# Optimization experiments

Measured on AMD Instinct MI355X. Metric: run time of the kernel, lower is better.

Reference implementation:

```python
import jax, jax.numpy as jnp
import numpy as np

EPS_LOG = 1e-07
EPS_LN = 1e-05


def layer_norm(x, gamma, beta):
    mu = jnp.mean(x, axis=-1, keepdims=True)
    var = jnp.mean((x - mu) ** 2, axis=-1, keepdims=True)
    return (x - mu) * jax.lax.rsqrt(var + EPS_LN) * gamma + beta


def setup_inputs() -> dict:
    key = jax.random.key(0)
    ks = jax.random.split(key, 20)
    N, D_IN, H = 500000, 39, 256
    inp = {"x": jax.random.uniform(ks[0], (N, D_IN), dtype=jnp.float32)}
    # fc1: 39 -> 256
    inp["W1"] = jax.random.normal(ks[1], (H, D_IN), dtype=jnp.float32) * (1.0 / np.sqrt(D_IN))
    inp["b1"] = jnp.zeros((H,), dtype=jnp.float32)
    # fc2..fc7: 256 -> 256
    for i in range(2, 8):
        inp[f"W{i}"] = jax.random.normal(ks[i], (H, H), dtype=jnp.float32) * (1.0 / np.sqrt(H))
        inp[f"b{i}"] = jnp.zeros((H,), dtype=jnp.float32)
    # fc8: 256 -> 1
    inp["W8"] = jax.random.normal(ks[8], (1, H), dtype=jnp.float32) * (1.0 / np.sqrt(H))
    inp["b8"] = jnp.zeros((1,), dtype=jnp.float32)
    # shared LayerNorm affine params
    inp["gamma"] = jnp.ones((H,), dtype=jnp.float32)
    inp["beta"] = jnp.zeros((H,), dtype=jnp.float32)
    return inp


def reference(x, W1, b1, W2, b2, W3, b3, W4, b4, W5, b5, W6, b6, W7, b7, W8, b8, gamma, beta):
    h = 0.1 * jnp.log(x + EPS_LOG)
    h = jnp.tanh(h @ W1.T + b1)
    for W, b in ((W2, b2), (W3, b3), (W4, b4), (W5, b5), (W6, b6), (W7, b7)):
        h = jax.nn.elu(layer_norm(h, gamma, beta) @ W.T + b)
    return layer_norm(h, gamma, beta) @ W8.T + b8
```

## Files before the change

kernel.cpp:

```cpp
#include <hip/hip_runtime.h>

typedef _Float16 f16;
typedef _Float16 f16x8 __attribute__((ext_vector_type(8)));
typedef float f32x4 __attribute__((ext_vector_type(4)));

#define N_ROWS 500000
#define EPS_LOG 1e-7f
#define EPS_LN  1e-5f

#define CST_BYTE_OFF 20480

__global__ void prep_kernel(const float* __restrict__ W1,
                            const float* __restrict__ W2, const float* __restrict__ W3,
                            const float* __restrict__ W4, const float* __restrict__ W5,
                            const float* __restrict__ W6, const float* __restrict__ W7,
                            const float* __restrict__ b2, const float* __restrict__ b3,
                            const float* __restrict__ b4, const float* __restrict__ b5,
                            const float* __restrict__ b6, const float* __restrict__ b7,
                            const float* __restrict__ gamma, const float* __restrict__ beta,
                            f16* __restrict__ ws) {
  float* cstF = (float*)((char*)ws + CST_BYTE_OFF);
  int idx = blockIdx.x * 256 + threadIdx.x;
  if (idx < 10240) {
    int j = idx / 40, k = idx - j * 40;
    ws[idx] = (f16)((k < 39) ? W1[j * 39 + k] : 0.0f);
  } else if (idx < 16384) {
  } else if (idx < 409600) {
    int o = idx - 16384;
    int li = o >> 16;  o &= 65535;
    const float* W = (li == 0) ? W2 : (li == 1) ? W3 : (li == 2) ? W4
                   : (li == 3) ? W5 : (li == 4) ? W6 : W7;
    int e = o & 7, j = (o >> 3) & 255, kgrp = (o >> 11) & 3, kt = o >> 13;
    int k = kt * 32 + kgrp * 8 + e;
    ws[idx] = (f16)(W[j * 256 + k] * gamma[k]);
  } else if (idx < 411136) {
    int o = idx - 409600;
    int li = o >> 8, j = o & 255;
    const float* W = (li == 0) ? W2 : (li == 1) ? W3 : (li == 2) ? W4
                   : (li == 3) ? W5 : (li == 4) ? W6 : W7;
    const float* b = (li == 0) ? b2 : (li == 1) ? b3 : (li == 2) ? b4
                   : (li == 3) ? b5 : (li == 4) ? b6 : b7;
    float sg = 0.f, bb = 0.f;
    for (int k = 0; k < 256; ++k) {
      float w = W[j * 256 + k];
      sg += w * gamma[k];
      bb += w * beta[k];
    }
    cstF[li * 256 + j] = sg;
    cstF[1536 + li * 256 + j] = bb + b[j];
  }
}

__global__ __launch_bounds__(256, 2)
void mlp_kernel(const float* __restrict__ x, const f16* __restrict__ wsw,
                const float* __restrict__ b1, const float* __restrict__ W8,
                const float* __restrict__ b8, const float* __restrict__ gamma,
                const float* __restrict__ beta, float* __restrict__ out) {
  __shared__ __attribute__((aligned(16))) f16 hbuf[128 * 256];
  __shared__ __attribute__((aligned(16))) f16 wslab[8192];

  const float* cstF = (const float*)((const char*)wsw + CST_BYTE_OFF);
  const int t = threadIdx.x;
  const int lane = t & 63;
  const int wid = t >> 6;
  const int lm = lane & 15;
  const int lg = lane >> 4;
  const long rowbase = (long)blockIdx.x * 128;
  const int R0 = wid * 32;
  const int myrow0 = R0 + lm;
  const int myrow1 = R0 + 16 + lm;
  const int sA0 = ((myrow0 >> 1) & 7) << 3;
  const int sA1 = ((myrow1 >> 1) & 7) << 3;

  f16x8 ld0, ld1, ld2, ld3;
  auto slab_load = [&](const f16* g) {
    ld0 = *(const f16x8*)(g + (0 * 256 + t) * 8);
    ld1 = *(const f16x8*)(g + (1 * 256 + t) * 8);
    ld2 = *(const f16x8*)(g + (2 * 256 + t) * 8);
    ld3 = *(const f16x8*)(g + (3 * 256 + t) * 8);
  };
  auto slab_write = [&]() {
    *(f16x8*)&wslab[(0 * 256 + t) * 8] = ld0;
    *(f16x8*)&wslab[(1 * 256 + t) * 8] = ld1;
    *(f16x8*)&wslab[(2 * 256 + t) * 8] = ld2;
    *(f16x8*)&wslab[(3 * 256 + t) * 8] = ld3;
  };

  const f16* WgBase = wsw + 16384;
  slab_load(WgBase);

  #pragma unroll 1
  for (int i = 0; i < 32; ++i) {
    int r = R0 + i;
    long gr = rowbase + r;
    float tv = 0.0f;
    if (lane < 39) {
      float xv = (gr < N_ROWS) ? x[gr * 39 + lane] : 1.0f;
      tv = 0.1f * __logf(xv + EPS_LOG);
    }
    hbuf[r * 256 + (lane ^ (((r >> 1) & 7) << 3))] = (f16)tv;
  }

  f32x4 acc0[16], acc1[16];

  auto do_tile = [&](f32x4* acc, int rbase, bool tanh_act, const float* cvec) {
    float nm[4] = {0, 0, 0, 0}, nq[4] = {0, 0, 0, 0};
    #pragma unroll
    for (int nt = 0; nt < 16; ++nt) {
      float c0 = cvec[nt * 16 + lm];
      #pragma unroll
      for (int i = 0; i < 4; ++i) {
        float v = acc[nt][i] + c0;
        float a;
        if (tanh_act) {
          float e2 = __expf(2.f * v);
          a = 1.f - 2.f / (e2 + 1.f);
        } else {
          a = (v > 0.f) ? v : (__expf(v) - 1.f);
        }
        acc[nt][i] = a;
        nm[i] += a;
        nq[i] = fmaf(a, a, nq[i]);
      }
    }
    #pragma unroll
    for (int off = 1; off < 16; off <<= 1) {
      #pragma unroll
      for (int i = 0; i < 4; ++i) {
        nm[i] += __shfl_xor(nm[i], off, 64);
        nq[i] += __shfl_xor(nq[i], off, 64);
      }
    }
    float mu[4], is_[4];
    #pragma unroll
    for (int i = 0; i < 4; ++i) {
      float m = nm[i] * (1.f / 256.f);
      float var = nq[i] * (1.f / 256.f) - m * m;
      mu[i] = m;
      is_[i] = rsqrtf(var + EPS_LN);
    }
    #pragma unroll
    for (int nt = 0; nt < 16; ++nt) {
      int col = nt * 16 + lm;
      #pragma unroll
      for (int i = 0; i < 4; ++i) {
        int r = rbase + lg * 4 + i;
        hbuf[r * 256 + (col ^ (((r >> 1) & 7) << 3))] =
            (f16)((acc[nt][i] - mu[i]) * is_[i]);
      }
    }
  };

  {
    #pragma unroll
    for (int i = 0; i < 16; ++i) { acc0[i] = (f32x4){0,0,0,0}; acc1[i] = (f32x4){0,0,0,0}; }
    #pragma unroll
    for (int kt = 0; kt < 2; ++kt) {
      f16x8 av0 = *(const f16x8*)&hbuf[myrow0 * 256 + ((kt * 32 + lg * 8) ^ sA0)];
      f16x8 av1 = *(const f16x8*)&hbuf[myrow1 * 256 + ((kt * 32 + lg * 8) ^ sA1)];
      #pragma unroll
      for (int nt = 0; nt < 16; ++nt) {
        int j40 = (nt * 16 + lm) * 40;
        f16x8 bf = 0;
        if (kt == 0)       bf = *(const f16x8*)&wsw[j40 + lg * 8];
        else if (lg == 0)  bf = *(const f16x8*)&wsw[j40 + 32];
        acc0[nt] = __builtin_amdgcn_mfma_f32_16x16x32_f16(av0, bf, acc0[nt], 0, 0, 0);
        acc1[nt] = __builtin_amdgcn_mfma_f32_16x16x32_f16(av1, bf, acc1[nt], 0, 0, 0);
      }
    }
    do_tile(acc0, R0,      true, b1);
    do_tile(acc1, R0 + 16, true, b1);
  }

  #pragma unroll 1
  for (int li = 0; li < 6; ++li) {
    #pragma unroll
    for (int i = 0; i < 16; ++i) { acc0[i] = (f32x4){0,0,0,0}; acc1[i] = (f32x4){0,0,0,0}; }
    #pragma unroll 1
    for (int kt = 0; kt < 8; ++kt) {
      slab_write();
      if (kt < 7)       slab_load(WgBase + li * 65536 + (kt + 1) * 8192);
      else if (li < 5)  slab_load(WgBase + (li + 1) * 65536);
      __syncthreads();
      {
        f16x8 av0 = *(const f16x8*)&hbuf[myrow0 * 256 + ((kt * 32 + lg * 8) ^ sA0)];
        f16x8 av1 = *(const f16x8*)&hbuf[myrow1 * 256 + ((kt * 32 + lg * 8) ^ sA1)];
        #pragma unroll
        for (int nt = 0; nt < 16; ++nt) {
          f16x8 bf = *(const f16x8*)&wslab[lg * 2048 + (nt * 16 + lm) * 8];
          acc0[nt] = __builtin_amdgcn_mfma_f32_16x16x32_f16(av0, bf, acc0[nt], 0, 0, 0);
          acc1[nt] = __builtin_amdgcn_mfma_f32_16x16x32_f16(av1, bf, acc1[nt], 0, 0, 0);
        }
      }
      __syncthreads();
    }
    do_tile(acc0, R0,      false, cstF + 1536 + li * 256);
    do_tile(acc1, R0 + 16, false, cstF + 1536 + li * 256);
  }

  {
    float wg8[16], be8 = 0.f;
    #pragma unroll
    for (int j = 0; j < 16; ++j) {
      int c = lm * 16 + j;
      float w = W8[c];
      wg8[j] = w * gamma[c];
      be8 = fmaf(w, beta[c], be8);
    }
    #pragma unroll
    for (int off = 1; off < 16; off <<= 1) be8 += __shfl_xor(be8, off, 64);
    float cb8 = be8 + b8[0];
    #pragma unroll
    for (int tile = 0; tile < 2; ++tile) {
      #pragma unroll
      for (int i = 0; i < 4; ++i) {
        int r = R0 + tile * 16 + lg * 4 + i;
        int s3 = ((r >> 1) & 7) << 3;
        f16x8 h0 = *(const f16x8*)&hbuf[r * 256 + ((lm * 16) ^ s3)];
        f16x8 h1 = *(const f16x8*)&hbuf[r * 256 + ((lm * 16 + 8) ^ s3)];
        float d = 0.f;
        #pragma unroll
        for (int j = 0; j < 8; ++j) d = fmaf((float)h0[j], wg8[j], d);
        #pragma unroll
        for (int j = 0; j < 8; ++j) d = fmaf((float)h1[j], wg8[8 + j], d);
        #pragma unroll
        for (int off = 1; off < 16; off <<= 1) d += __shfl_xor(d, off, 64);
        if (lm == 0) {
          long gr = rowbase + r;
          if (gr < N_ROWS) out[gr] = d + cb8;
        }
      }
    }
  }
}

extern "C" void kernel_launch(void* const* d_in, const int* in_sizes, int n_in,
                              void* d_out, int out_size, void* d_ws, size_t ws_size,
                              hipStream_t stream) {
  const float* x  = (const float*)d_in[0];
  const float* W1 = (const float*)d_in[1];
  const float* b1 = (const float*)d_in[2];
  const float* W2 = (const float*)d_in[3];
  const float* b2 = (const float*)d_in[4];
  const float* W3 = (const float*)d_in[5];
  const float* b3 = (const float*)d_in[6];
  const float* W4 = (const float*)d_in[7];
  const float* b4 = (const float*)d_in[8];
  const float* W5 = (const float*)d_in[9];
  const float* b5 = (const float*)d_in[10];
  const float* W6 = (const float*)d_in[11];
  const float* b6 = (const float*)d_in[12];
  const float* W7 = (const float*)d_in[13];
  const float* b7 = (const float*)d_in[14];
  const float* W8 = (const float*)d_in[15];
  const float* b8 = (const float*)d_in[16];
  const float* gm = (const float*)d_in[17];
  const float* bt = (const float*)d_in[18];
  f16* ws = (f16*)d_ws;
  float* out = (float*)d_out;

  prep_kernel<<<1606, 256, 0, stream>>>(W1, W2, W3, W4, W5, W6, W7,
                                        b2, b3, b4, b5, b6, b7, gm, bt, ws);

  int nblk = (N_ROWS + 127) / 128;
  mlp_kernel<<<nblk, 256, 0, stream>>>(x, ws, b1, W8, b8, gm, bt, out);
}
```

Before: 1.034 ms.

## Transpose MFMA operands so LayerNorm stats reduce per-lane and fuse final projection

```diff
diff --git a/kernel.cpp b/kernel.cpp
--- a/kernel.cpp
+++ b/kernel.cpp
@@ -1,6 +1,7 @@
 #include <hip/hip_runtime.h>
 
 typedef _Float16 f16;
+typedef _Float16 f16x4 __attribute__((ext_vector_type(4)));
 typedef _Float16 f16x8 __attribute__((ext_vector_type(8)));
 typedef float f32x4 __attribute__((ext_vector_type(4)));
 
@@ -14,6 +15,7 @@
                             const float* __restrict__ W2, const float* __restrict__ W3,
                             const float* __restrict__ W4, const float* __restrict__ W5,
                             const float* __restrict__ W6, const float* __restrict__ W7,
+                            const float* __restrict__ W8, const float* __restrict__ b8,
                             const float* __restrict__ b2, const float* __restrict__ b3,
                             const float* __restrict__ b4, const float* __restrict__ b5,
                             const float* __restrict__ b6, const float* __restrict__ b7,
@@ -40,22 +42,27 @@
                    : (li == 3) ? W5 : (li == 4) ? W6 : W7;
     const float* b = (li == 0) ? b2 : (li == 1) ? b3 : (li == 2) ? b4
                    : (li == 3) ? b5 : (li == 4) ? b6 : b7;
-    float sg = 0.f, bb = 0.f;
+    float bb = 0.f;
+    for (int k = 0; k < 256; ++k) bb = fmaf(W[j * 256 + k], beta[k], bb);
+    cstF[1536 + li * 256 + j] = bb + b[j];
+  } else if (idx < 411392) {
+    int j = idx - 411136;
+    cstF[j] = W8[j] * gamma[j];
+  } else if (idx == 411392) {
+    float s8 = 0.f, cb = 0.f;
     for (int k = 0; k < 256; ++k) {
-      float w = W[j * 256 + k];
-      sg += w * gamma[k];
-      bb += w * beta[k];
-    }
-    cstF[li * 256 + j] = sg;
-    cstF[1536 + li * 256 + j] = bb + b[j];
+      float w = W8[k];
+      s8 = fmaf(w, gamma[k], s8);
+      cb = fmaf(w, beta[k], cb);
+    }
+    cstF[256] = s8;
+    cstF[257] = cb + b8[0];
   }
 }
 
-__global__ __launch_bounds__(256, 2)
+__global__ __launch_bounds__(256, 1)
 void mlp_kernel(const float* __restrict__ x, const f16* __restrict__ wsw,
-                const float* __restrict__ b1, const float* __restrict__ W8,
-                const float* __restrict__ b8, const float* __restrict__ gamma,
-                const float* __restrict__ beta, float* __restrict__ out) {
+                const float* __restrict__ b1, float* __restrict__ out) {
   __shared__ __attribute__((aligned(16))) f16 hbuf[128 * 256];
   __shared__ __attribute__((aligned(16))) f16 wslab[8192];
 
@@ -67,10 +74,10 @@
   const int lg = lane >> 4;
   const long rowbase = (long)blockIdx.x * 128;
   const int R0 = wid * 32;
-  const int myrow0 = R0 + lm;
-  const int myrow1 = R0 + 16 + lm;
-  const int sA0 = ((myrow0 >> 1) & 7) << 3;
-  const int sA1 = ((myrow1 >> 1) & 7) << 3;
+  const int row0 = R0 + lm;
+  const int row1 = R0 + 16 + lm;
+  const int sw0 = (row0 & 7) << 3;
+  const int sw1 = (row1 & 7) << 3;
 
   f16x8 ld0, ld1, ld2, ld3;
   auto slab_load = [&](const f16* g) {
@@ -98,19 +105,19 @@
       float xv = (gr < N_ROWS) ? x[gr * 39 + lane] : 1.0f;
       tv = 0.1f * __logf(xv + EPS_LOG);
     }
-    hbuf[r * 256 + (lane ^ (((r >> 1) & 7) << 3))] = (f16)tv;
+    hbuf[r * 256 + (lane ^ ((r & 7) << 3))] = (f16)tv;
   }
 
   f32x4 acc0[16], acc1[16];
 
-  auto do_tile = [&](f32x4* acc, int rbase, bool tanh_act, const float* cvec) {
-    float nm[4] = {0, 0, 0, 0}, nq[4] = {0, 0, 0, 0};
-    #pragma unroll
-    for (int nt = 0; nt < 16; ++nt) {
-      float c0 = cvec[nt * 16 + lm];
+  auto do_tile = [&](f32x4* acc, int rt, bool tanh_act, const float* cvec) {
+    float nm = 0.f, nq = 0.f;
+    #pragma unroll
+    for (int jt = 0; jt < 16; ++jt) {
+      f32x4 c4 = *(const f32x4*)&cvec[jt * 16 + lg * 4];
       #pragma unroll
       for (int i = 0; i < 4; ++i) {
-        float v = acc[nt][i] + c0;
+        float v = acc[jt][i] + c4[i];
         float a;
         if (tanh_act) {
           float e2 = __expf(2.f * v);
@@ -118,36 +125,52 @@
         } else {
           a = (v > 0.f) ? v : (__expf(v) - 1.f);
         }
-        acc[nt][i] = a;
-        nm[i] += a;
-        nq[i] = fmaf(a, a, nq[i]);
-      }
-    }
-    #pragma unroll
-    for (int off = 1; off < 16; off <<= 1) {
+        acc[jt][i] = a;
+        nm += a;
+        nq = fmaf(a, a, nq);
+      }
+    }
+    nm += __shfl_xor(nm, 16, 64);  nq += __shfl_xor(nq, 16, 64);
+    nm += __shfl_xor(nm, 32, 64);  nq += __shfl_xor(nq, 32, 64);
+    float mu = nm * (1.f / 256.f);
+    float is = rsqrtf(nq * (1.f / 256.f) - mu * mu + EPS_LN);
+    int row = R0 + rt * 16 + lm;
+    int sw = (row & 7) << 3;
+    #pragma unroll
+    for (int jt = 0; jt < 16; ++jt) {
+      f16x4 z4;
+      #pragma unroll
+      for (int i = 0; i < 4; ++i) z4[i] = (f16)((acc[jt][i] - mu) * is);
+      *(f16x4*)&hbuf[row * 256 + ((jt * 16 + lg * 4) ^ sw)] = z4;
+    }
+  };
+
+  auto final_tile = [&](f32x4* acc, int rt) {
+    const float* bb7 = cstF + 1536 + 5 * 256;
+    float s8 = cstF[256], cb8 = cstF[257];
+    float nm = 0.f, nq = 0.f, dt = 0.f;
+    #pragma unroll
+    for (int jt = 0; jt < 16; ++jt) {
+      f32x4 c4 = *(const f32x4*)&bb7[jt * 16 + lg * 4];
+      f32x4 w4 = *(const f32x4*)&cstF[jt * 16 + lg * 4];
       #pragma unroll
       for (int i = 0; i < 4; ++i) {
-        nm[i] += __shfl_xor(nm[i], off, 64);
-        nq[i] += __shfl_xor(nq[i], off, 64);
-      }
-    }
-    float mu[4], is_[4];
-    #pragma unroll
-    for (int i = 0; i < 4; ++i) {
-      float m = nm[i] * (1.f / 256.f);
-      float var = nq[i] * (1.f / 256.f) - m * m;
-      mu[i] = m;
-      is_[i] = rsqrtf(var + EPS_LN);
-    }
-    #pragma unroll
-    for (int nt = 0; nt < 16; ++nt) {
-      int col = nt * 16 + lm;
-      #pragma unroll
-      for (int i = 0; i < 4; ++i) {
-        int r = rbase + lg * 4 + i;
-        hbuf[r * 256 + (col ^ (((r >> 1) & 7) << 3))] =
-            (f16)((acc[nt][i] - mu[i]) * is_[i]);
-      }
+        float v = acc[jt][i] + c4[i];
+        float a = (v > 0.f) ? v : (__expf(v) - 1.f);
+        nm += a;
+        nq = fmaf(a, a, nq);
+        dt = fmaf(a, w4[i], dt);
+      }
+    }
+    nm += __shfl_xor(nm, 16, 64);  nq += __shfl_xor(nq, 16, 64);
+    dt += __shfl_xor(dt, 16, 64);
+    nm += __shfl_xor(nm, 32, 64);  nq += __shfl_xor(nq, 32, 64);
+    dt += __shfl_xor(dt, 32, 64);
+    float mu = nm * (1.f / 256.f);
+    float is = rsqrtf(nq * (1.f / 256.f) - mu * mu + EPS_LN);
+    if (lane < 16) {
+      long gr = rowbase + R0 + rt * 16 + lm;
+      if (gr < N_ROWS) out[gr] = fmaf(is, dt - mu * s8, cb8);
     }
   };
 
@@ -156,20 +179,20 @@
     for (int i = 0; i < 16; ++i) { acc0[i] = (f32x4){0,0,0,0}; acc1[i] = (f32x4){0,0,0,0}; }
     #pragma unroll
     for (int kt = 0; kt < 2; ++kt) {
-      f16x8 av0 = *(const f16x8*)&hbuf[myrow0 * 256 + ((kt * 32 + lg * 8) ^ sA0)];
-      f16x8 av1 = *(const f16x8*)&hbuf[myrow1 * 256 + ((kt * 32 + lg * 8) ^ sA1)];
-      #pragma unroll
-      for (int nt = 0; nt < 16; ++nt) {
-        int j40 = (nt * 16 + lm) * 40;
-        f16x8 bf = 0;
-        if (kt == 0)       bf = *(const f16x8*)&wsw[j40 + lg * 8];
-        else if (lg == 0)  bf = *(const f16x8*)&wsw[j40 + 32];
-        acc0[nt] = __builtin_amdgcn_mfma_f32_16x16x32_f16(av0, bf, acc0[nt], 0, 0, 0);
-        acc1[nt] = __builtin_amdgcn_mfma_f32_16x16x32_f16(av1, bf, acc1[nt], 0, 0, 0);
-      }
-    }
-    do_tile(acc0, R0,      true, b1);
-    do_tile(acc1, R0 + 16, true, b1);
+      f16x8 bv0 = *(const f16x8*)&hbuf[row0 * 256 + ((kt * 32 + lg * 8) ^ sw0)];
+      f16x8 bv1 = *(const f16x8*)&hbuf[row1 * 256 + ((kt * 32 + lg * 8) ^ sw1)];
+      #pragma unroll
+      for (int jt = 0; jt < 16; ++jt) {
+        int j40 = (jt * 16 + lm) * 40;
+        f16x8 af = 0;
+        if (kt == 0)       af = *(const f16x8*)&wsw[j40 + lg * 8];
+        else if (lg == 0)  af = *(const f16x8*)&wsw[j40 + 32];
+        acc0[jt] = __builtin_amdgcn_mfma_f32_16x16x32_f16(af, bv0, acc0[jt], 0, 0, 0);
+        acc1[jt] = __builtin_amdgcn_mfma_f32_16x16x32_f16(af, bv1, acc1[jt], 0, 0, 0);
+      }
+    }
+    do_tile(acc0, 0, true, b1);
+    do_tile(acc1, 1, true, b1);
   }
 
   #pragma unroll 1
@@ -183,53 +206,23 @@
       else if (li < 5)  slab_load(WgBase + (li + 1) * 65536);
       __syncthreads();
       {
-        f16x8 av0 = *(const f16x8*)&hbuf[myrow0 * 256 + ((kt * 32 + lg * 8) ^ sA0)];
-        f16x8 av1 = *(const f16x8*)&hbuf[myrow1 * 256 + ((kt * 32 + lg * 8) ^ sA1)];
+        f16x8 bv0 = *(const f16x8*)&hbuf[row0 * 256 + ((kt * 32 + lg * 8) ^ sw0)];
+        f16x8 bv1 = *(const f16x8*)&hbuf[row1 * 256 + ((kt * 32 + lg * 8) ^ sw1)];
         #pragma unroll
-        for (int nt = 0; nt < 16; ++nt) {
-          f16x8 bf = *(const f16x8*)&wslab[lg * 2048 + (nt * 16 + lm) * 8];
-          acc0[nt] = __builtin_amdgcn_mfma_f32_16x16x32_f16(av0, bf, acc0[nt], 0, 0, 0);
-          acc1[nt] = __builtin_amdgcn_mfma_f32_16x16x32_f16(av1, bf, acc1[nt], 0, 0, 0);
+        for (int jt = 0; jt < 16; ++jt) {
+          f16x8 af = *(const f16x8*)&wslab[lg * 2048 + (jt * 16 + lm) * 8];
+          acc0[jt] = __builtin_amdgcn_mfma_f32_16x16x32_f16(af, bv0, acc0[jt], 0, 0, 0);
+          acc1[jt] = __builtin_amdgcn_mfma_f32_16x16x32_f16(af, bv1, acc1[jt], 0, 0, 0);
         }
       }
       __syncthreads();
     }
-    do_tile(acc0, R0,      false, cstF + 1536 + li * 256);
-    do_tile(acc1, R0 + 16, false, cstF + 1536 + li * 256);
-  }
-
-  {
-    float wg8[16], be8 = 0.f;
-    #pragma unroll
-    for (int j = 0; j < 16; ++j) {
-      int c = lm * 16 + j;
-      float w = W8[c];
-      wg8[j] = w * gamma[c];
-      be8 = fmaf(w, beta[c], be8);
-    }
-    #pragma unroll
-    for (int off = 1; off < 16; off <<= 1) be8 += __shfl_xor(be8, off, 64);
-    float cb8 = be8 + b8[0];
-    #pragma unroll
-    for (int tile = 0; tile < 2; ++tile) {
-      #pragma unroll
-      for (int i = 0; i < 4; ++i) {
-        int r = R0 + tile * 16 + lg * 4 + i;
-        int s3 = ((r >> 1) & 7) << 3;
-        f16x8 h0 = *(const f16x8*)&hbuf[r * 256 + ((lm * 16) ^ s3)];
-        f16x8 h1 = *(const f16x8*)&hbuf[r * 256 + ((lm * 16 + 8) ^ s3)];
-        float d = 0.f;
-        #pragma unroll
-        for (int j = 0; j < 8; ++j) d = fmaf((float)h0[j], wg8[j], d);
-        #pragma unroll
-        for (int j = 0; j < 8; ++j) d = fmaf((float)h1[j], wg8[8 + j], d);
-        #pragma unroll
-        for (int off = 1; off < 16; off <<= 1) d += __shfl_xor(d, off, 64);
-        if (lm == 0) {
-          long gr = rowbase + r;
-          if (gr < N_ROWS) out[gr] = d + cb8;
-        }
-      }
+    if (li < 5) {
+      do_tile(acc0, 0, false, cstF + 1536 + li * 256);
+      do_tile(acc1, 1, false, cstF + 1536 + li * 256);
+    } else {
+      final_tile(acc0, 0);
+      final_tile(acc1, 1);
     }
   }
 }
@@ -259,9 +252,9 @@
   f16* ws = (f16*)d_ws;
   float* out = (float*)d_out;
 
-  prep_kernel<<<1606, 256, 0, stream>>>(W1, W2, W3, W4, W5, W6, W7,
+  prep_kernel<<<1608, 256, 0, stream>>>(W1, W2, W3, W4, W5, W6, W7, W8, b8,
                                         b2, b3, b4, b5, b6, b7, gm, bt, ws);
 
   int nblk = (N_ROWS + 127) / 128;
-  mlp_kernel<<<nblk, 256, 0, stream>>>(x, ws, b1, W8, b8, gm, bt, out);
+  mlp_kernel<<<nblk, 256, 0, stream>>>(x, ws, b1, out);
 }
```

After: 1.390 ms. +34.5%, slower.
